# Performance work log

Hardware: AMD Instinct MI355X
Metric: run time of the kernel (lower is better)

## Reference

```python
import jax, jax.numpy as jnp
import numpy as np
from functools import partial

B, D, H, T = 1024, 512, 1024, 64  # batch, latent dim, MLP hidden, time points


def setup_inputs() -> dict:
    key = jax.random.key(0)
    k0, k1, k2, k3, k4 = jax.random.split(key, 5)
    z0 = jax.random.normal(k0, (B, D), dtype=jnp.float32)
    # strictly increasing time grid, modest dt for a stable tanh-MLP vector field
    t = jnp.arange(T, dtype=jnp.float32) * 0.02
    # 2-layer tanh MLP ode_func: dz/dt = tanh(z @ W1 + b1) @ W2 + b2
    W1 = jax.random.normal(k1, (D, H), dtype=jnp.float32) * (1.0 / np.sqrt(D))
    b1 = jnp.zeros((H,), dtype=jnp.float32)
    W2 = jax.random.normal(k2, (H, D), dtype=jnp.float32) * (1.0 / np.sqrt(H))
    b2 = jnp.zeros((D,), dtype=jnp.float32)
    return {"z0": z0, "t": t, "W1": W1, "b1": b1, "W2": W2, "b2": b2}


def _ode_func(z, W1, b1, W2, b2):
    # autonomous latent vector field: [B, D] -> [B, D]
    return jnp.tanh(z @ W1 + b1) @ W2 + b2


def reference(z0, t, W1, b1, W2, b2):
    """odeint(ode_func, z0, t, method='rk4'): one classical RK4 step per interval.
    Returns trajectory [T, B, D] with traj[0] == z0 (torchdiffeq convention)."""
    f = partial(_ode_func, W1=W1, b1=b1, W2=W2, b2=b2)
    dts = t[1:] - t[:-1]  # [T-1]

    def step(z, dt):
        k1 = f(z)
        k2 = f(z + 0.5 * dt * k1)
        k3 = f(z + 0.5 * dt * k2)
        k4 = f(z + dt * k3)
        z_new = z + (dt / 6.0) * (k1 + 2.0 * k2 + 2.0 * k3 + k4)
        return z_new, z_new

    _, traj = jax.lax.scan(step, z0, dts)  # [T-1, B, D]
    return jnp.concatenate([z0[None], traj], axis=0)  # [T, B, D]
```

## Files before the change

### kernel.cpp

```cpp
#include <hip/hip_runtime.h>
#include <hip/hip_bf16.h>

#define BATCH 1024
#define DLAT  512
#define HHID  1024
#define TPTS  64
#define BD    (BATCH * DLAT)

#define NBLK 256
#define NTHR 512
#define RGN  16


typedef __attribute__((ext_vector_type(8))) short short8;
typedef __attribute__((ext_vector_type(4))) float f32x4;

__device__ __forceinline__ short f2bf(float x) {
    __hip_bfloat16 h = __float2bfloat16(x);
    return __builtin_bit_cast(short, h);
}
__device__ __forceinline__ float fast_tanh(float x) {
    x = fminf(9.f, fmaxf(-9.f, x));
    const float e = __expf(2.f * x);
    return (e - 1.f) / (e + 1.f);
}

__device__ __forceinline__ void rg_barrier(int* flg, int cg, int target, int tid)
{
    __syncthreads();
    if (tid == 0) atomicAdd(flg + cg * 4, 1);
    if (tid < 16) {
        const int* fp = flg + tid * 4;
        int v;
        do {
            v = __hip_atomic_load(fp, __ATOMIC_RELAXED,
                                  __HIP_MEMORY_SCOPE_AGENT);
            if (!__all(v >= target)) __builtin_amdgcn_s_sleep(2);
            else break;
        } while (true);
    }
    __syncthreads();
    asm volatile("buffer_inv\n\ts_waitcnt vmcnt(0)" ::: "memory");
}

__global__ __launch_bounds__(NTHR) void ode_coop(
    const float* __restrict__ z0, const float* __restrict__ t,
    const float* __restrict__ W1, const float* __restrict__ b1,
    const float* __restrict__ W2, const float* __restrict__ b2,
    short* __restrict__ zf, short* __restrict__ Hf,
    int* __restrict__ fl, int* __restrict__ xcnt,
    float* __restrict__ traj)
{
    __shared__ __align__(16) short W1L[4 * 16 * 64 * 8];
    __shared__ __align__(16) short W2L[2 * 32 * 64 * 8];
    __shared__ float b1L[64];
    __shared__ float b2L[32];
    __shared__ int slotS;

    const int tid  = threadIdx.x;
    const int lane = tid & 63;
    const int w    = tid >> 6;
    const int q    = lane >> 4;
    const int cl   = lane & 15;

    unsigned int xcc;
    asm("s_getreg_b32 %0, hwreg(HW_REG_XCC_ID)" : "=s"(xcc));
    xcc &= 7u;
    if (tid == 0) slotS = atomicAdd(&xcnt[xcc], 1);
    __syncthreads();
    const int slot = slotS & 31;
    const int rg   = (int)xcc * 2 + (slot >> 4);
    const int cg   = slot & 15;
    int* flg = fl + rg * 64;

    for (int i = tid; i < 4 * 16 * 64; i += NTHR) {
        const int ct = i >> 10, kt = (i >> 6) & 15, l = i & 63;
        const int k0 = kt * 32 + (l >> 4) * 8;
        const int n  = cg * 64 + ct * 16 + (l & 15);
        short8 v;
#pragma unroll
        for (int j = 0; j < 8; ++j) v[j] = f2bf(W1[(size_t)(k0 + j) * HHID + n]);
        *(short8*)&W1L[i * 8] = v;
    }
    for (int i = tid; i < 2 * 32 * 64; i += NTHR) {
        const int ct = i >> 11, kt = (i >> 6) & 31, l = i & 63;
        const int k0 = kt * 32 + (l >> 4) * 8;
        const int n  = cg * 32 + ct * 16 + (l & 15);
        short8 v;
#pragma unroll
        for (int j = 0; j < 8; ++j) v[j] = f2bf(W2[(size_t)(k0 + j) * DLAT + n]);
        *(short8*)&W2L[i * 8] = v;
    }
    if (tid < 64)      b1L[tid]      = b1[cg * 64 + tid];
    else if (tid < 96) b2L[tid - 64] = b2[cg * 32 + (tid - 64)];

    const int rt   = w >> 1;
    const int c0   = (w & 1) * 2;
    const int ct2b = w & 1;
    const int rowb = rg * 64 + rt * 16 + q * 4;
    const int nb   = cg * 32 + ct2b * 16 + cl;
    const int clb  = ct2b * 16 + cl;

    const size_t zbase = ((size_t)(rg * 4 + rt) * 16 + cg) * 512 +
                         (size_t)(((clb >> 3) * 16 + q * 4) * 8 + (clb & 7));
    size_t hbase[2];
#pragma unroll
    for (int c = 0; c < 2; ++c) {
        const int colc = (c0 + c) * 16 + cl;
        hbase[c] = ((size_t)(rg * 4 + rt) * 32 + cg * 2 + (colc >> 5)) * 512 +
                   (size_t)((((colc & 31) >> 3) * 16 + q * 4) * 8 + (colc & 7));
    }

    float zreg[4], kacc[4];
#pragma unroll
    for (int reg = 0; reg < 4; ++reg) {
        const float zv = z0[(size_t)(rowb + reg) * DLAT + nb];
        zreg[reg] = zv;
        traj[(size_t)(rowb + reg) * DLAT + nb] = zv;
        zf[zbase + reg * 8] = f2bf(zv);
    }

    int target = 0;
    target += 1; rg_barrier(flg, cg, target, tid);

    const short* zrow = zf + (size_t)(rg * 4 + rt) * 8192  + lane * 8;
    const short* hrow = Hf + (size_t)(rg * 4 + rt) * 16384 + lane * 8;
    const short* w1p  = &W1L[c0 * 8192 + lane * 8];
    const short* w2p  = &W2L[ct2b * 16384 + lane * 8];

    for (int step = 0; step < TPTS - 1; ++step) {
        const float dt = t[step + 1] - t[step];

        if (step > 0) {
#pragma unroll
            for (int reg = 0; reg < 4; ++reg)
                traj[(size_t)step * BD + (size_t)(rowb + reg) * DLAT + nb] =
                    zreg[reg];
        }

#pragma unroll
        for (int stage = 0; stage < 4; ++stage) {
            {
                f32x4 acc0 = {0.f, 0.f, 0.f, 0.f};
                f32x4 acc1 = {0.f, 0.f, 0.f, 0.f};
#pragma unroll
                for (int kt = 0; kt < 16; ++kt) {
                    const short8 a  = *(const short8*)(zrow + kt * 512);
                    const short8 bA = *(const short8*)(w1p + kt * 512);
                    const short8 bB = *(const short8*)(w1p + 8192 + kt * 512);
                    acc0 = __builtin_amdgcn_mfma_f32_16x16x32_bf16(a, bA, acc0, 0, 0, 0);
                    acc1 = __builtin_amdgcn_mfma_f32_16x16x32_bf16(a, bB, acc1, 0, 0, 0);
                }
#pragma unroll
                for (int c = 0; c < 2; ++c) {
                    const int   cloc = (c0 + c) * 16 + cl;
                    const float bb   = b1L[cloc];
                    const f32x4 av   = c ? acc1 : acc0;
#pragma unroll
                    for (int reg = 0; reg < 4; ++reg)
                        Hf[hbase[c] + reg * 8] = f2bf(fast_tanh(av[reg] + bb));
                }
            }
            target += 1; rg_barrier(flg, cg, target, tid);

            {
                f32x4 acce = {0.f, 0.f, 0.f, 0.f};
                f32x4 acco = {0.f, 0.f, 0.f, 0.f};
#pragma unroll
                for (int kt = 0; kt < 32; kt += 2) {
                    const short8 a0  = *(const short8*)(hrow + kt * 512);
                    const short8 a1  = *(const short8*)(hrow + kt * 512 + 512);
                    const short8 bb0 = *(const short8*)(w2p + kt * 512);
                    const short8 bb1 = *(const short8*)(w2p + kt * 512 + 512);
                    acce = __builtin_amdgcn_mfma_f32_16x16x32_bf16(a0, bb0, acce, 0, 0, 0);
                    acco = __builtin_amdgcn_mfma_f32_16x16x32_bf16(a1, bb1, acco, 0, 0, 0);
                }
                const float bb = b2L[clb];
#pragma unroll
                for (int reg = 0; reg < 4; ++reg) {
                    const float kv = acce[reg] + acco[reg] + bb;
                    float znext;
                    if (stage == 0) {
                        kacc[reg] = kv;        znext = zreg[reg] + 0.5f * dt * kv;
                    } else if (stage == 1) {
                        kacc[reg] += 2.f * kv; znext = zreg[reg] + 0.5f * dt * kv;
                    } else if (stage == 2) {
                        kacc[reg] += 2.f * kv; znext = zreg[reg] + dt * kv;
                    } else {
                        zreg[reg] += (dt * (1.f / 6.f)) * (kacc[reg] + kv);
                        znext = zreg[reg];
                    }
                    zf[zbase + reg * 8] = f2bf(znext);
                }
            }
            target += 1; rg_barrier(flg, cg, target, tid);
        }
    }

#pragma unroll
    for (int reg = 0; reg < 4; ++reg)
        traj[(size_t)(TPTS - 1) * BD + (size_t)(rowb + reg) * DLAT + nb] =
            zreg[reg];
}

extern "C" void kernel_launch(void* const* d_in, const int* in_sizes, int n_in,
                              void* d_out, int out_size, void* d_ws, size_t ws_size,
                              hipStream_t stream)
{
    (void)in_sizes; (void)n_in; (void)out_size; (void)ws_size;

    const float* z0 = (const float*)d_in[0];
    const float* t  = (const float*)d_in[1];
    const float* W1 = (const float*)d_in[2];
    const float* b1 = (const float*)d_in[3];
    const float* W2 = (const float*)d_in[4];
    const float* b2 = (const float*)d_in[5];
    float*       traj = (float*)d_out;

    short* zf   = (short*)d_ws;
    short* Hf   = (short*)((char*)d_ws + (1u << 20));
    int*   fl   = (int*)((char*)d_ws + (3u << 20));
    int*   xcnt = (int*)((char*)d_ws + (3u << 20) + 4096);

    hipMemsetAsync(fl, 0, 4096 + 32, stream);

    void* args[] = {&z0, &t, &W1, &b1, &W2, &b2, &zf, &Hf, &fl, &xcnt, &traj};
    hipLaunchCooperativeKernel((const void*)ode_coop, dim3(NBLK), dim3(NTHR),
                               args, 0, stream);
}
```

Measured before the change: 1.408 ms.

## Split work across 512 cooperative blocks with K-split second GEMM

Adds a 512-block variant in which each block owns half as many output columns. The second GEMM is split along K across wave pairs, and the partial sums are reduced through shared memory. The group barrier now spans 32 blocks, and the launch falls back to a 256-block kernel, whose barrier is simplified to a single shared counter, when occupancy is too low. The aim is to run two blocks per CU so more CUs and waves hide latency. In exchange, each barrier has twice as many participants and needs an extra intra-block sync per stage.

Measured after the change: 1.665 ms. 18.2% more time.

```diff
diff --git a/kernel.cpp b/kernel.cpp
--- a/kernel.cpp
+++ b/kernel.cpp
@@ -7,9 +7,7 @@
 #define TPTS  64
 #define BD    (BATCH * DLAT)
 
-#define NBLK 256
 #define NTHR 512
-#define RGN  16
 
 
 typedef __attribute__((ext_vector_type(8))) short short8;
@@ -25,30 +23,26 @@
     return (e - 1.f) / (e + 1.f);
 }
 
-__device__ __forceinline__ void rg_barrier(int* flg, int cg, int target, int tid)
+__device__ __forceinline__ void rg_barrier16(int* bar, int cidx, int target, int tid)
 {
     __syncthreads();
-    if (tid == 0) atomicAdd(flg + cg * 4, 1);
-    if (tid < 16) {
-        const int* fp = flg + tid * 4;
-        int v;
-        do {
-            v = __hip_atomic_load(fp, __ATOMIC_RELAXED,
-                                  __HIP_MEMORY_SCOPE_AGENT);
-            if (!__all(v >= target)) __builtin_amdgcn_s_sleep(2);
-            else break;
-        } while (true);
+    if (tid == 0) {
+        atomicAdd(&bar[cidx], 1);
+        while (__hip_atomic_load(&bar[cidx], __ATOMIC_RELAXED,
+                                 __HIP_MEMORY_SCOPE_AGENT) < target) {
+            __builtin_amdgcn_s_sleep(2);
+        }
     }
     __syncthreads();
     asm volatile("buffer_inv\n\ts_waitcnt vmcnt(0)" ::: "memory");
 }
 
-__global__ __launch_bounds__(NTHR) void ode_coop(
+__global__ __launch_bounds__(NTHR) void ode_coop256(
     const float* __restrict__ z0, const float* __restrict__ t,
     const float* __restrict__ W1, const float* __restrict__ b1,
     const float* __restrict__ W2, const float* __restrict__ b2,
     short* __restrict__ zf, short* __restrict__ Hf,
-    int* __restrict__ fl, int* __restrict__ xcnt,
+    int* __restrict__ bar, int* __restrict__ xcnt,
     float* __restrict__ traj)
 {
     __shared__ __align__(16) short W1L[4 * 16 * 64 * 8];
@@ -71,7 +65,7 @@
     const int slot = slotS & 31;
     const int rg   = (int)xcc * 2 + (slot >> 4);
     const int cg   = slot & 15;
-    int* flg = fl + rg * 64;
+    const int cidx = rg * 32;
 
     for (int i = tid; i < 4 * 16 * 64; i += NTHR) {
         const int ct = i >> 10, kt = (i >> 6) & 15, l = i & 63;
@@ -121,7 +115,7 @@
     }
 
     int target = 0;
-    target += 1; rg_barrier(flg, cg, target, tid);
+    target += 1; rg_barrier16(bar, cidx, target, tid);
 
     const short* zrow = zf + (size_t)(rg * 4 + rt) * 8192  + lane * 8;
     const short* hrow = Hf + (size_t)(rg * 4 + rt) * 16384 + lane * 8;
@@ -130,14 +124,12 @@
 
     for (int step = 0; step < TPTS - 1; ++step) {
         const float dt = t[step + 1] - t[step];
-
         if (step > 0) {
 #pragma unroll
             for (int reg = 0; reg < 4; ++reg)
                 traj[(size_t)step * BD + (size_t)(rowb + reg) * DLAT + nb] =
                     zreg[reg];
         }
-
 #pragma unroll
         for (int stage = 0; stage < 4; ++stage) {
             {
@@ -161,7 +153,7 @@
                         Hf[hbase[c] + reg * 8] = f2bf(fast_tanh(av[reg] + bb));
                 }
             }
-            target += 1; rg_barrier(flg, cg, target, tid);
+            target += 1; rg_barrier16(bar, cidx, target, tid);
 
             {
                 f32x4 acce = {0.f, 0.f, 0.f, 0.f};
@@ -193,14 +185,186 @@
                     zf[zbase + reg * 8] = f2bf(znext);
                 }
             }
-            target += 1; rg_barrier(flg, cg, target, tid);
-        }
-    }
-
+            target += 1; rg_barrier16(bar, cidx, target, tid);
+        }
+    }
 #pragma unroll
     for (int reg = 0; reg < 4; ++reg)
         traj[(size_t)(TPTS - 1) * BD + (size_t)(rowb + reg) * DLAT + nb] =
             zreg[reg];
+}
+
+__device__ __forceinline__ void rg_barrier32(int* flg, int cg, int target, int tid)
+{
+    __syncthreads();
+    if (tid == 0) atomicAdd(flg + cg * 4, 1);
+    if (tid < 32) {
+        const int* fp = flg + tid * 4;
+        int v;
+        do {
+            v = __hip_atomic_load(fp, __ATOMIC_RELAXED,
+                                  __HIP_MEMORY_SCOPE_AGENT);
+            if (!__all(v >= target)) __builtin_amdgcn_s_sleep(2);
+            else break;
+        } while (true);
+    }
+    __syncthreads();
+    asm volatile("buffer_inv\n\ts_waitcnt vmcnt(0)" ::: "memory");
+}
+
+__global__ __launch_bounds__(NTHR) void ode_coop512(
+    const float* __restrict__ z0, const float* __restrict__ t,
+    const float* __restrict__ W1, const float* __restrict__ b1,
+    const float* __restrict__ W2, const float* __restrict__ b2,
+    short* __restrict__ zf, short* __restrict__ Hf,
+    int* __restrict__ fl, int* __restrict__ xcnt,
+    float* __restrict__ traj)
+{
+    __shared__ __align__(16) short W1L[2 * 16 * 64 * 8];
+    __shared__ __align__(16) short W2L[32 * 64 * 8];
+    __shared__ float Rbuf[4 * 64 * 4];
+    __shared__ float b1L[32];
+    __shared__ float b2L[16];
+    __shared__ int slotS;
+
+    const int tid  = threadIdx.x;
+    const int lane = tid & 63;
+    const int w    = tid >> 6;
+    const int q    = lane >> 4;
+    const int cl   = lane & 15;
+
+    unsigned int xcc;
+    asm("s_getreg_b32 %0, hwreg(HW_REG_XCC_ID)" : "=s"(xcc));
+    xcc &= 7u;
+    if (tid == 0) slotS = atomicAdd(&xcnt[xcc], 1);
+    __syncthreads();
+    const int slot = slotS & 63;
+    const int rg   = (int)xcc * 2 + (slot >> 5);
+    const int cg   = slot & 31;
+    int* flg = fl + rg * 128;
+
+    for (int i = tid; i < 2 * 16 * 64; i += NTHR) {
+        const int ct = i >> 10, kt = (i >> 6) & 15, l = i & 63;
+        const int k0 = kt * 32 + (l >> 4) * 8;
+        const int n  = cg * 32 + ct * 16 + (l & 15);
+        short8 v;
+#pragma unroll
+        for (int j = 0; j < 8; ++j) v[j] = f2bf(W1[(size_t)(k0 + j) * HHID + n]);
+        *(short8*)&W1L[i * 8] = v;
+    }
+    for (int i = tid; i < 32 * 64; i += NTHR) {
+        const int kt = i >> 6, l = i & 63;
+        const int k0 = kt * 32 + (l >> 4) * 8;
+        const int n  = cg * 16 + (l & 15);
+        short8 v;
+#pragma unroll
+        for (int j = 0; j < 8; ++j) v[j] = f2bf(W2[(size_t)(k0 + j) * DLAT + n]);
+        *(short8*)&W2L[i * 8] = v;
+    }
+    if (tid < 32)      b1L[tid]      = b1[cg * 32 + tid];
+    else if (tid < 48) b2L[tid - 32] = b2[cg * 16 + (tid - 32)];
+
+    const int rt    = w >> 1;
+    const int ct    = w & 1;
+    const int khalf = w & 1;
+
+    const int hloc = ct * 16 + cl;
+    const size_t hAbase = ((size_t)(rg * 4 + rt) * 32 + cg) * 512 +
+                          (size_t)(((q * 4) | (((hloc >> 3) & 3) << 4)) * 8 + (hloc & 7));
+    const int zloc = (cg & 1) * 16 + cl;
+    const size_t zbase = ((size_t)(rg * 4 + rt) * 16 + (cg >> 1)) * 512 +
+                         (size_t)(((q * 4) | (((zloc >> 3) & 3) << 4)) * 8 + (zloc & 7));
+    const int rowb = rg * 64 + rt * 16 + q * 4;
+    const int nb   = cg * 16 + cl;
+
+    float zreg[4], kacc[4];
+    if (khalf == 0) {
+#pragma unroll
+        for (int reg = 0; reg < 4; ++reg) {
+            const float zv = z0[(size_t)(rowb + reg) * DLAT + nb];
+            zreg[reg] = zv;
+            traj[(size_t)(rowb + reg) * DLAT + nb] = zv;
+            zf[zbase + reg * 8] = f2bf(zv);
+        }
+    }
+
+    int target = 0;
+    target += 1; rg_barrier32(flg, cg, target, tid);
+
+    const short* zrow = zf + (size_t)(rg * 4 + rt) * 8192  + lane * 8;
+    const short* hrow = Hf + (size_t)(rg * 4 + rt) * 16384 + lane * 8;
+    const short* w1p  = &W1L[ct * 8192 + lane * 8];
+    const short* w2p  = &W2L[khalf * 16 * 512 + lane * 8];
+
+    for (int step = 0; step < TPTS - 1; ++step) {
+        const float dt = t[step + 1] - t[step];
+        if (step > 0 && khalf == 0) {
+#pragma unroll
+            for (int reg = 0; reg < 4; ++reg)
+                traj[(size_t)step * BD + (size_t)(rowb + reg) * DLAT + nb] =
+                    zreg[reg];
+        }
+#pragma unroll
+        for (int stage = 0; stage < 4; ++stage) {
+            {
+                f32x4 acc = {0.f, 0.f, 0.f, 0.f};
+#pragma unroll
+                for (int kt = 0; kt < 16; ++kt) {
+                    const short8 a = *(const short8*)(zrow + kt * 512);
+                    const short8 b = *(const short8*)(w1p + kt * 512);
+                    acc = __builtin_amdgcn_mfma_f32_16x16x32_bf16(a, b, acc, 0, 0, 0);
+                }
+                const float bb = b1L[hloc];
+#pragma unroll
+                for (int reg = 0; reg < 4; ++reg)
+                    Hf[hAbase + reg * 8] = f2bf(fast_tanh(acc[reg] + bb));
+            }
+            target += 1; rg_barrier32(flg, cg, target, tid);
+
+            {
+                f32x4 acc = {0.f, 0.f, 0.f, 0.f};
+#pragma unroll
+                for (int kt = 0; kt < 16; ++kt) {
+                    const short8 a = *(const short8*)(hrow + (khalf * 16 + kt) * 512);
+                    const short8 b = *(const short8*)(w2p + kt * 512);
+                    acc = __builtin_amdgcn_mfma_f32_16x16x32_bf16(a, b, acc, 0, 0, 0);
+                }
+                if (khalf == 1) {
+#pragma unroll
+                    for (int reg = 0; reg < 4; ++reg)
+                        Rbuf[(rt * 64 + lane) * 4 + reg] = acc[reg];
+                }
+                __syncthreads();
+                if (khalf == 0) {
+                    const float bb = b2L[cl];
+#pragma unroll
+                    for (int reg = 0; reg < 4; ++reg) {
+                        const float kv = acc[reg] +
+                                         Rbuf[(rt * 64 + lane) * 4 + reg] + bb;
+                        float znext;
+                        if (stage == 0) {
+                            kacc[reg] = kv;        znext = zreg[reg] + 0.5f * dt * kv;
+                        } else if (stage == 1) {
+                            kacc[reg] += 2.f * kv; znext = zreg[reg] + 0.5f * dt * kv;
+                        } else if (stage == 2) {
+                            kacc[reg] += 2.f * kv; znext = zreg[reg] + dt * kv;
+                        } else {
+                            zreg[reg] += (dt * (1.f / 6.f)) * (kacc[reg] + kv);
+                            znext = zreg[reg];
+                        }
+                        zf[zbase + reg * 8] = f2bf(znext);
+                    }
+                }
+            }
+            target += 1; rg_barrier32(flg, cg, target, tid);
+        }
+    }
+    if (khalf == 0) {
+#pragma unroll
+        for (int reg = 0; reg < 4; ++reg)
+            traj[(size_t)(TPTS - 1) * BD + (size_t)(rowb + reg) * DLAT + nb] =
+                zreg[reg];
+    }
 }
 
 extern "C" void kernel_launch(void* const* d_in, const int* in_sizes, int n_in,
@@ -217,14 +381,26 @@
     const float* b2 = (const float*)d_in[5];
     float*       traj = (float*)d_out;
 
-    short* zf   = (short*)d_ws;
-    short* Hf   = (short*)((char*)d_ws + (1u << 20));
-    int*   fl   = (int*)((char*)d_ws + (3u << 20));
-    int*   xcnt = (int*)((char*)d_ws + (3u << 20) + 4096);
-
-    hipMemsetAsync(fl, 0, 4096 + 32, stream);
-
-    void* args[] = {&z0, &t, &W1, &b1, &W2, &b2, &zf, &Hf, &fl, &xcnt, &traj};
-    hipLaunchCooperativeKernel((const void*)ode_coop, dim3(NBLK), dim3(NTHR),
-                               args, 0, stream);
-}
+    short* zf    = (short*)d_ws;
+    short* Hf    = (short*)((char*)d_ws + (1u << 20));
+    int*   fl    = (int*)((char*)d_ws + (3u << 20));
+    int*   xcntA = (int*)((char*)d_ws + (3u << 20) + 8192);
+    int*   xcntB = (int*)((char*)d_ws + (3u << 20) + 8192 + 32);
+
+    hipMemsetAsync(fl, 0, 8192 + 64, stream);
+
+    int nb = 1;
+    (void)hipOccupancyMaxActiveBlocksPerMultiprocessor(&nb, ode_coop512, NTHR, 0);
+
+    hipError_t e = hipErrorUnknown;
+    if (nb >= 2) {
+        void* argsA[] = {&z0, &t, &W1, &b1, &W2, &b2, &zf, &Hf, &fl, &xcntA, &traj};
+        e = hipLaunchCooperativeKernel((const void*)ode_coop512, dim3(512),
+                                       dim3(NTHR), argsA, 0, stream);
+    }
+    if (nb < 2 || e != hipSuccess) {
+        void* argsB[] = {&z0, &t, &W1, &b1, &W2, &b2, &zf, &Hf, &fl, &xcntB, &traj};
+        hipLaunchCooperativeKernel((const void*)ode_coop256, dim3(256),
+                                   dim3(NTHR), argsB, 0, stream);
+    }
+}
```
